# Performance work log

Measured on AMD Instinct MI355X. Metric: run time of the kernel, lower is better.

The kernel has to match this reference:

```python
import jax, jax.numpy as jnp
import numpy as np

N = 100000   # nodes
D = 128      # in_ft == out_ft (residual mix requires equality)
E = 1600000  # edges (nnz of sparse A)


def setup_inputs() -> dict:
    key = jax.random.key(0)
    ks = jax.random.split(key, 8)
    X = jax.random.normal(ks[0], (N, D), dtype=jnp.float32)   # unused by forward math, kept for fidelity
    X0 = jax.random.normal(ks[1], (N, D), dtype=jnp.float32)
    row = jnp.sort(jax.random.randint(ks[2], (E,), 0, N))      # sparse A row indices (sorted)
    col = jax.random.randint(ks[3], (E,), 0, N)                # sparse A col indices
    vals = jax.random.uniform(ks[4], (E,), dtype=jnp.float32)  # sparse A values
    # nn.Linear(D, D): weight [out, in], bias [out]
    bound = 1.0 / np.sqrt(D)
    W = jax.random.uniform(ks[5], (D, D), minval=-bound, maxval=bound, dtype=jnp.float32)
    b = jax.random.uniform(ks[6], (D,), minval=-bound, maxval=bound, dtype=jnp.float32)
    alpha = jax.random.uniform(ks[7], (), dtype=jnp.float32)
    beta = jax.random.uniform(jax.random.fold_in(key, 7), (), dtype=jnp.float32)
    return {"X": X, "X0": X0, "row": row, "col": col, "vals": vals,
            "W": W, "b": b, "alpha": alpha, "beta": beta}


def reference(X, X0, row, col, vals, W, b, alpha, beta):
    # SpMM: (A @ X0)[i] = sum_e vals[e] * X0[col[e]] for edges with row[e] == i
    AX0 = jax.ops.segment_sum(vals[:, None] * X0[col], row, num_segments=N)  # [N, D]
    Xi = (1.0 - alpha) * AX0 + alpha * X0
    out = (1.0 - beta) * Xi + beta * (Xi @ W.T + b)
    return out
```

## Files before the change

kernel.cpp:

```cpp
#include <hip/hip_runtime.h>

#define D_FT 128

__device__ inline unsigned f2bf(float f) {
    unsigned u = __float_as_uint(f);
    return (u + 0x7FFFu + ((u >> 16) & 1u)) >> 16;
}
__device__ inline unsigned pack2bf(float a, float b) {
    return f2bf(a) | (f2bf(b) << 16);
}
__device__ inline float bf_lo(unsigned u) { return __uint_as_float(u << 16); }
__device__ inline float bf_hi(unsigned u) { return __uint_as_float(u & 0xFFFF0000u); }
__device__ inline float bf_us(unsigned short u) { return __uint_as_float((unsigned)u << 16); }

typedef __attribute__((ext_vector_type(4))) float f32x4;
typedef __attribute__((ext_vector_type(8))) short bf16x8;
union bf8u { bf16x8 v; unsigned u[4]; };

__global__ __launch_bounds__(256) void convert_x0_kernel(
    const float* __restrict__ X0, unsigned* __restrict__ xb, int n4)
{
    const int i = blockIdx.x * 256 + threadIdx.x;
    if (i < n4) {
        const float4 x = ((const float4*)X0)[i];
        uint2 v; v.x = pack2bf(x.x, x.y); v.y = pack2bf(x.z, x.w);
        ((uint2*)xb)[i] = v;
    }
}

__global__ __launch_bounds__(256) void build_row_ptr_kernel(
    const int* __restrict__ row, int* __restrict__ ptr, int n_edges, int n_nodes)
{
    const int e = blockIdx.x * 256 + threadIdx.x;
    if (e > n_edges) return;
    const int lo = (e == 0) ? 0 : row[e - 1] + 1;
    const int hi = (e == n_edges) ? n_nodes : row[e];
    for (int i = lo; i <= hi; ++i) ptr[i] = e;
}

__global__ __launch_bounds__(512) void fused_spmm_gemm_kernel(
    const unsigned* __restrict__ X0b,
    const int*      __restrict__ col,
    const float*    __restrict__ vals,
    const int*      __restrict__ row_ptr,
    const float*    __restrict__ W,
    const float*    __restrict__ bias,
    const float*    __restrict__ alpha_p,
    const float*    __restrict__ beta_p,
    float*          __restrict__ out,
    int n_nodes)
{
    __shared__ __align__(16) char lds_raw[65536];
    char* __restrict__ ldsXi = lds_raw;
    char* __restrict__ ldsW  = lds_raw + 32768;

    const int t    = threadIdx.x;
    const int wid  = t >> 6;
    const int lane = t & 63;
    const int bn   = blockIdx.x * 128;
    const float alpha = *alpha_p;

    for (int i = 0; i < 16; ++i) {
        const int nl   = wid * 16 + i;
        const int node = bn + nl;
        unsigned xw = 0;
        if (node < n_nodes) {
            const int ebeg = row_ptr[node];
            const int eend = row_ptr[node + 1];
            float ax = 0.f, ay = 0.f;
            for (int e = ebeg; e < eend; e += 64) {
                const int n = min(64, eend - e);
                int cl = 0; float vl = 0.f;
                if (lane < n) { cl = col[e + lane]; vl = vals[e + lane]; }
                for (int j0 = 0; j0 < n; j0 += 16) {
                    float vv[16]; unsigned xs[16];
                    #pragma unroll
                    for (int j = 0; j < 16; ++j) {
                        const int c = __shfl(cl, j0 + j);
                        vv[j] = __shfl(vl, j0 + j);
                        xs[j] = X0b[c * 64 + lane];
                    }
                    #pragma unroll
                    for (int j = 0; j < 16; ++j) {
                        ax += vv[j] * bf_lo(xs[j]);
                        ay += vv[j] * bf_hi(xs[j]);
                    }
                }
            }
            const unsigned s = X0b[node * 64 + lane];
            xw = pack2bf((1.f - alpha) * ax + alpha * bf_lo(s),
                         (1.f - alpha) * ay + alpha * bf_hi(s));
        }
        int byte = nl * 256 + lane * 4;
        byte ^= (nl & 7) << 4;
        *(unsigned*)(ldsXi + byte) = xw;
    }

    #pragma unroll
    for (int i = 0; i < 8; ++i) {
        const int f4 = i * 512 + t;
        const int o  = f4 >> 5;
        const int c4 = f4 & 31;
        const float4 x = *(const float4*)(W + (size_t)o * D_FT + c4 * 4);
        uint2 v; v.x = pack2bf(x.x, x.y); v.y = pack2bf(x.z, x.w);
        int byte = o * 256 + c4 * 8;
        byte ^= (o & 7) << 4;
        *(uint2*)(ldsW + byte) = v;
    }
    __syncthreads();

    const int llo = lane & 15;
    const int lhi = lane >> 4;

    bf16x8 a[4];
    #pragma unroll
    for (int ks = 0; ks < 4; ++ks) {
        const int r = wid * 16 + llo;
        int byte = r * 256 + ks * 64 + lhi * 16;
        byte ^= (r & 7) << 4;
        a[ks] = *(const bf16x8*)(ldsXi + byte);
    }

    f32x4 acc[8];
    #pragma unroll
    for (int n = 0; n < 8; ++n) acc[n] = (f32x4){0.f, 0.f, 0.f, 0.f};

    #pragma unroll
    for (int ks = 0; ks < 4; ++ks) {
        const int kb = ks * 64 + lhi * 16;
        #pragma unroll
        for (int n = 0; n < 8; ++n) {
            const int o = n * 16 + llo;
            int byte = o * 256 + kb;
            byte ^= (o & 7) << 4;
            const bf16x8 b = *(const bf16x8*)(ldsW + byte);
            acc[n] = __builtin_amdgcn_mfma_f32_16x16x32_bf16(a[ks], b, acc[n], 0, 0, 0);
        }
    }

    const float beta = *beta_p;
    const float ob = 1.f - beta;
    float bb[8];
    #pragma unroll
    for (int n = 0; n < 8; ++n) bb[n] = bias[n * 16 + llo];

    #pragma unroll
    for (int q = 0; q < 4; ++q) {
        const int rl = wid * 16 + lhi * 4 + q;
        const int R  = bn + rl;
        if (R < n_nodes) {
            #pragma unroll
            for (int n = 0; n < 8; ++n) {
                const int C = n * 16 + llo;
                int byte = rl * 256 + C * 2;
                byte ^= (rl & 7) << 4;
                const float xi = bf_us(*(const unsigned short*)(ldsXi + byte));
                out[(size_t)R * D_FT + C] = ob * xi + beta * (acc[n][q] + bb[n]);
            }
        }
    }
}

template<bool PTR>
__global__ __launch_bounds__(256) void spmm_mix_kernel(
    const float* __restrict__ X0,
    const int*   __restrict__ row,
    const int*   __restrict__ col,
    const float* __restrict__ vals,
    const int*   __restrict__ row_ptr,
    const float* __restrict__ alpha_p,
    float*       __restrict__ Xi,
    int n_nodes, int n_edges)
{
    const int wave = threadIdx.x >> 6;
    const int lane = threadIdx.x & 63;
    const int node = blockIdx.x * 4 + wave;
    if (node >= n_nodes) return;

    int ebeg, eend;
    if (PTR) {
        ebeg = row_ptr[node];
        eend = row_ptr[node + 1];
    } else {
        int lo0 = 0, hi0 = n_edges, lo1 = 0, hi1 = n_edges;
        while ((lo0 < hi0) || (lo1 < hi1)) {
            int m0 = (lo0 + hi0) >> 1; if (m0 >= n_edges) m0 = n_edges - 1;
            int m1 = (lo1 + hi1) >> 1; if (m1 >= n_edges) m1 = n_edges - 1;
            const int r0v = row[m0];
            const int r1v = row[m1];
            if (lo0 < hi0) { if (r0v < node)     lo0 = m0 + 1; else hi0 = m0; }
            if (lo1 < hi1) { if (r1v < node + 1) lo1 = m1 + 1; else hi1 = m1; }
        }
        ebeg = lo0; eend = lo1;
    }

    const int d0 = lane * 2;
    float ax = 0.f, ay = 0.f;

    for (int e = ebeg; e < eend; e += 64) {
        const int n = min(64, eend - e);
        int cl = 0; float vl = 0.f;
        if (lane < n) { cl = col[e + lane]; vl = vals[e + lane]; }
        for (int j0 = 0; j0 < n; j0 += 16) {
            float2 xs[16]; float vv[16];
            #pragma unroll
            for (int j = 0; j < 16; ++j) {
                const int c = __shfl(cl, j0 + j);
                vv[j] = __shfl(vl, j0 + j);
                xs[j] = *(const float2*)(X0 + (size_t)c * D_FT + d0);
            }
            #pragma unroll
            for (int j = 0; j < 16; ++j) {
                ax += vv[j] * xs[j].x;
                ay += vv[j] * xs[j].y;
            }
        }
    }

    const float alpha = *alpha_p;
    const float2 x0self = *(const float2*)(X0 + (size_t)node * D_FT + d0);
    float2 xi;
    xi.x = (1.f - alpha) * ax + alpha * x0self.x;
    xi.y = (1.f - alpha) * ay + alpha * x0self.y;
    *(float2*)(Xi + (size_t)node * D_FT + d0) = xi;
}

__global__ __launch_bounds__(256) void gemm_mix_f32_kernel(
    const float* __restrict__ W,
    const float* __restrict__ bias,
    const float* __restrict__ beta_p,
    float*       __restrict__ io,
    int n_nodes)
{
    __shared__ __align__(16) char lds_raw[32768];
    char*  __restrict__ ldsB = lds_raw;
    float* __restrict__ ldsS = (float*)lds_raw;

    const int t   = threadIdx.x;
    const int w   = t >> 6;
    const int l   = t & 63;
    const int lhi = l >> 4;
    const int llo = l & 15;
    const int r0  = blockIdx.x * 64;

    int arow = r0 + w * 16 + llo;
    if (arow >= n_nodes) arow = n_nodes - 1;
    const float* aptr = io + (size_t)arow * D_FT;
    float4 af0[4], af1[4];
    #pragma unroll
    for (int ks = 0; ks < 4; ++ks) {
        const int k0 = ks * 32 + lhi * 8;
        af0[ks] = *(const float4*)(aptr + k0);
        af1[ks] = *(const float4*)(aptr + k0 + 4);
    }

    #pragma unroll
    for (int i = 0; i < 16; ++i) {
        const int f4 = i * 256 + t;
        const int o  = f4 >> 5;
        const int c4 = f4 & 31;
        const float4 x = *(const float4*)(W + (size_t)o * D_FT + c4 * 4);
        uint2 v; v.x = pack2bf(x.x, x.y); v.y = pack2bf(x.z, x.w);
        int byte = o * 256 + c4 * 8;
        byte ^= (o & 7) << 4;
        *(uint2*)(ldsB + byte) = v;
    }
    __syncthreads();

    f32x4 acc[8];
    #pragma unroll
    for (int n = 0; n < 8; ++n) acc[n] = (f32x4){0.f, 0.f, 0.f, 0.f};

    #pragma unroll
    for (int ks = 0; ks < 4; ++ks) {
        bf8u a;
        a.u[0] = pack2bf(af0[ks].x, af0[ks].y);
        a.u[1] = pack2bf(af0[ks].z, af0[ks].w);
        a.u[2] = pack2bf(af1[ks].x, af1[ks].y);
        a.u[3] = pack2bf(af1[ks].z, af1[ks].w);
        const int kb = ks * 64 + lhi * 16;
        #pragma unroll
        for (int n = 0; n < 8; ++n) {
            const int o = n * 16 + llo;
            int byte = o * 256 + kb;
            byte ^= (o & 7) << 4;
            const bf16x8 b = *(const bf16x8*)(ldsB + byte);
            acc[n] = __builtin_amdgcn_mfma_f32_16x16x32_bf16(a.v, b, acc[n], 0, 0, 0);
        }
    }

    __syncthreads();
    #pragma unroll
    for (int n = 0; n < 8; ++n) {
        const int C = n * 16 + llo;
        const int rt = w * 16 + lhi * 4;
        #pragma unroll
        for (int q = 0; q < 4; ++q)
            ldsS[(rt + q) * 128 + C] = acc[n][q];
    }
    __syncthreads();

    const float beta = *beta_p;
    const float ob = 1.f - beta;
    const int c4 = t & 31;
    const int rb = t >> 5;
    const float4 bb = *(const float4*)(bias + c4 * 4);

    #pragma unroll
    for (int i = 0; i < 8; ++i) {
        const int r  = rb * 8 + i;
        const int gr = r0 + r;
        if (gr < n_nodes) {
            const float4 a4  = *(const float4*)(ldsS + r * 128 + c4 * 4);
            const float4 xi4 = *(const float4*)(io + (size_t)gr * D_FT + c4 * 4);
            float4 o;
            o.x = ob * xi4.x + beta * (a4.x + bb.x);
            o.y = ob * xi4.y + beta * (a4.y + bb.y);
            o.z = ob * xi4.z + beta * (a4.z + bb.z);
            o.w = ob * xi4.w + beta * (a4.w + bb.w);
            *(float4*)(io + (size_t)gr * D_FT + c4 * 4) = o;
        }
    }
}

extern "C" void kernel_launch(void* const* d_in, const int* in_sizes, int n_in,
                              void* d_out, int out_size, void* d_ws, size_t ws_size,
                              hipStream_t stream) {
    const float* X0    = (const float*)d_in[1];
    const int*   row   = (const int*)  d_in[2];
    const int*   col   = (const int*)  d_in[3];
    const float* vals  = (const float*)d_in[4];
    const float* W     = (const float*)d_in[5];
    const float* b     = (const float*)d_in[6];
    const float* alpha = (const float*)d_in[7];
    const float* beta  = (const float*)d_in[8];
    float* out = (float*)d_out;

    const int n_nodes = in_sizes[1] / D_FT;
    const int n_edges = in_sizes[2];

    const size_t ptr_bytes = (size_t)(n_nodes + 1) * sizeof(int);
    const size_t BFOFF = 524288;
    const size_t BFSZ  = (size_t)n_nodes * 256;
    const bool ptr_ok = (ws_size >= ptr_bytes);
    const bool fused  = ptr_ok && (ws_size >= BFOFF + BFSZ) && (BFOFF >= ptr_bytes);

    if (fused) {
        int*      row_ptr = (int*)d_ws;
        unsigned* X0b     = (unsigned*)((char*)d_ws + BFOFF);
        build_row_ptr_kernel<<<(n_edges + 256) / 256, 256, 0, stream>>>(
            row, row_ptr, n_edges, n_nodes);
        const int n4 = n_nodes * D_FT / 4;
        convert_x0_kernel<<<(n4 + 255) / 256, 256, 0, stream>>>(X0, X0b, n4);
        fused_spmm_gemm_kernel<<<(n_nodes + 127) / 128, 512, 0, stream>>>(
            X0b, col, vals, row_ptr, W, b, alpha, beta, out, n_nodes);
    } else if (ptr_ok) {
        int* row_ptr = (int*)d_ws;
        build_row_ptr_kernel<<<(n_edges + 256) / 256, 256, 0, stream>>>(
            row, row_ptr, n_edges, n_nodes);
        spmm_mix_kernel<true><<<(n_nodes + 3) / 4, 256, 0, stream>>>(
            X0, row, col, vals, row_ptr, alpha, out, n_nodes, n_edges);
        gemm_mix_f32_kernel<<<(n_nodes + 63) / 64, 256, 0, stream>>>(
            W, b, beta, out, n_nodes);
    } else {
        spmm_mix_kernel<false><<<(n_nodes + 3) / 4, 256, 0, stream>>>(
            X0, row, col, vals, nullptr, alpha, out, n_nodes, n_edges);
        gemm_mix_f32_kernel<<<(n_nodes + 63) / 64, 256, 0, stream>>>(
            W, b, beta, out, n_nodes);
    }
}
```

Before: 252.2 us.

## Merge prep kernels, pre-convert W to bf16, read W fragments from global

Folds the row-pointer build, the X0 bf16 conversion and a new W bf16 conversion into one prep kernel, dropping one launch. The fused SpMM+GEMM kernel no longer stages W in LDS; each wave reads bf16 W fragments straight from global/L2. This halves LDS use per block to 32 KB and adds a min-blocks hint to launch_bounds, so more blocks can be resident to hide gather latency. The cost is repeated global/L2 reads of W by every wave, plus a larger workspace requirement for the fused path.

```diff
diff --git a/kernel.cpp b/kernel.cpp
--- a/kernel.cpp
+++ b/kernel.cpp
@@ -17,8 +17,10 @@
 typedef __attribute__((ext_vector_type(8))) short bf16x8;
 union bf8u { bf16x8 v; unsigned u[4]; };
 
-__global__ __launch_bounds__(256) void convert_x0_kernel(
-    const float* __restrict__ X0, unsigned* __restrict__ xb, int n4)
+__global__ __launch_bounds__(256) void prep_kernel(
+    const float* __restrict__ X0, unsigned* __restrict__ xb, int n4,
+    const float* __restrict__ W,  unsigned* __restrict__ wb, int n4w,
+    const int* __restrict__ row,  int* __restrict__ ptr, int n_edges, int n_nodes)
 {
     const int i = blockIdx.x * 256 + threadIdx.x;
     if (i < n4) {
@@ -26,33 +28,31 @@
         uint2 v; v.x = pack2bf(x.x, x.y); v.y = pack2bf(x.z, x.w);
         ((uint2*)xb)[i] = v;
     }
-}
-
-__global__ __launch_bounds__(256) void build_row_ptr_kernel(
-    const int* __restrict__ row, int* __restrict__ ptr, int n_edges, int n_nodes)
-{
-    const int e = blockIdx.x * 256 + threadIdx.x;
-    if (e > n_edges) return;
-    const int lo = (e == 0) ? 0 : row[e - 1] + 1;
-    const int hi = (e == n_edges) ? n_nodes : row[e];
-    for (int i = lo; i <= hi; ++i) ptr[i] = e;
-}
-
-__global__ __launch_bounds__(512) void fused_spmm_gemm_kernel(
+    if (i < n4w) {
+        const float4 x = ((const float4*)W)[i];
+        uint2 v; v.x = pack2bf(x.x, x.y); v.y = pack2bf(x.z, x.w);
+        ((uint2*)wb)[i] = v;
+    }
+    if (i <= n_edges) {
+        const int lo = (i == 0) ? 0 : row[i - 1] + 1;
+        const int hi = (i == n_edges) ? n_nodes : row[i];
+        for (int k = lo; k <= hi; ++k) ptr[k] = i;
+    }
+}
+
+__global__ __launch_bounds__(512, 8) void fused_spmm_gemm_kernel(
     const unsigned* __restrict__ X0b,
+    const unsigned* __restrict__ Wb,
     const int*      __restrict__ col,
     const float*    __restrict__ vals,
     const int*      __restrict__ row_ptr,
-    const float*    __restrict__ W,
     const float*    __restrict__ bias,
     const float*    __restrict__ alpha_p,
     const float*    __restrict__ beta_p,
     float*          __restrict__ out,
     int n_nodes)
 {
-    __shared__ __align__(16) char lds_raw[65536];
-    char* __restrict__ ldsXi = lds_raw;
-    char* __restrict__ ldsW  = lds_raw + 32768;
+    __shared__ __align__(16) char ldsXi[32768];
 
     const int t    = threadIdx.x;
     const int wid  = t >> 6;
@@ -95,18 +95,6 @@
         byte ^= (nl & 7) << 4;
         *(unsigned*)(ldsXi + byte) = xw;
     }
-
-    #pragma unroll
-    for (int i = 0; i < 8; ++i) {
-        const int f4 = i * 512 + t;
-        const int o  = f4 >> 5;
-        const int c4 = f4 & 31;
-        const float4 x = *(const float4*)(W + (size_t)o * D_FT + c4 * 4);
-        uint2 v; v.x = pack2bf(x.x, x.y); v.y = pack2bf(x.z, x.w);
-        int byte = o * 256 + c4 * 8;
-        byte ^= (o & 7) << 4;
-        *(uint2*)(ldsW + byte) = v;
-    }
     __syncthreads();
 
     const int llo = lane & 15;
@@ -125,15 +113,13 @@
     #pragma unroll
     for (int n = 0; n < 8; ++n) acc[n] = (f32x4){0.f, 0.f, 0.f, 0.f};
 
-    #pragma unroll
-    for (int ks = 0; ks < 4; ++ks) {
-        const int kb = ks * 64 + lhi * 16;
+    const char* wbase = (const char*)Wb + llo * 256 + lhi * 16;
+    #pragma unroll
+    for (int n = 0; n < 8; ++n) {
+        const char* wrow = wbase + n * 16 * 256;
         #pragma unroll
-        for (int n = 0; n < 8; ++n) {
-            const int o = n * 16 + llo;
-            int byte = o * 256 + kb;
-            byte ^= (o & 7) << 4;
-            const bf16x8 b = *(const bf16x8*)(ldsW + byte);
+        for (int ks = 0; ks < 4; ++ks) {
+            const bf16x8 b = *(const bf16x8*)(wrow + ks * 64);
             acc[n] = __builtin_amdgcn_mfma_f32_16x16x32_bf16(a[ks], b, acc[n], 0, 0, 0);
         }
     }
@@ -323,6 +309,16 @@
     }
 }
 
+__global__ __launch_bounds__(256) void build_row_ptr_kernel(
+    const int* __restrict__ row, int* __restrict__ ptr, int n_edges, int n_nodes)
+{
+    const int e = blockIdx.x * 256 + threadIdx.x;
+    if (e > n_edges) return;
+    const int lo = (e == 0) ? 0 : row[e - 1] + 1;
+    const int hi = (e == n_edges) ? n_nodes : row[e];
+    for (int i = lo; i <= hi; ++i) ptr[i] = e;
+}
+
 extern "C" void kernel_launch(void* const* d_in, const int* in_sizes, int n_in,
                               void* d_out, int out_size, void* d_ws, size_t ws_size,
                               hipStream_t stream) {
@@ -342,18 +338,24 @@
     const size_t ptr_bytes = (size_t)(n_nodes + 1) * sizeof(int);
     const size_t BFOFF = 524288;
     const size_t BFSZ  = (size_t)n_nodes * 256;
+    const size_t WBSZ  = (size_t)D_FT * D_FT * 2;
     const bool ptr_ok = (ws_size >= ptr_bytes);
-    const bool fused  = ptr_ok && (ws_size >= BFOFF + BFSZ) && (BFOFF >= ptr_bytes);
+    const bool fused  = ptr_ok && (ws_size >= BFOFF + BFSZ + WBSZ)
+                               && (BFOFF >= ptr_bytes);
 
     if (fused) {
         int*      row_ptr = (int*)d_ws;
         unsigned* X0b     = (unsigned*)((char*)d_ws + BFOFF);
-        build_row_ptr_kernel<<<(n_edges + 256) / 256, 256, 0, stream>>>(
-            row, row_ptr, n_edges, n_nodes);
-        const int n4 = n_nodes * D_FT / 4;
-        convert_x0_kernel<<<(n4 + 255) / 256, 256, 0, stream>>>(X0, X0b, n4);
+        unsigned* Wbf     = (unsigned*)((char*)d_ws + BFOFF + BFSZ);
+        const int n4  = n_nodes * D_FT / 4;
+        const int n4w = D_FT * D_FT / 4;
+        int span = n4;
+        if (n_edges + 1 > span) span = n_edges + 1;
+        if (n4w > span) span = n4w;
+        prep_kernel<<<(span + 255) / 256, 256, 0, stream>>>(
+            X0, X0b, n4, W, Wbf, n4w, row, row_ptr, n_edges, n_nodes);
         fused_spmm_gemm_kernel<<<(n_nodes + 127) / 128, 512, 0, stream>>>(
-            X0b, col, vals, row_ptr, W, b, alpha, beta, out, n_nodes);
+            X0b, Wbf, col, vals, row_ptr, b, alpha, beta, out, n_nodes);
     } else if (ptr_ok) {
         int* row_ptr = (int*)d_ws;
         build_row_ptr_kernel<<<(n_edges + 256) / 256, 256, 0, stream>>>(
```

Result: slower. 258.4 us (+2.4%).
